# Kernel optimization log

Measured on AMD Instinct MI355X. Metric: run time of the kernel, lower is better.

Reference implementation:

```python
import jax, jax.numpy as jnp
import numpy as np

# Minimal Mamba (alxndrTL mamba.py style) as used by MambaLithium.
# d_model=512, d_inner=1024 (expand=2), d_state=16, d_conv=4, dt_rank=32, n_layers=4.

EPS = 1e-5

def rmsnorm(x, w):
    # x: (B,L,D), w: (D,)
    return x * jax.lax.rsqrt(jnp.mean(x * x, axis=-1, keepdims=True) + EPS) * w

def causal_depthwise_conv(x, w, b):
    # x: (B,L,ED), w: (ED,K), b: (ED,)
    ED, K = w.shape
    xc = jnp.swapaxes(x, 1, 2)                       # (B,ED,L)
    k = w[:, None, :]                                # (ED,1,K) OIH
    y = jax.lax.conv_general_dilated(
        xc, k, window_strides=(1,), padding=[(K - 1, 0)],
        dimension_numbers=('NCH', 'OIH', 'NCH'), feature_group_count=ED)
    return jnp.swapaxes(y + b[None, :, None], 1, 2)  # (B,L,ED)

def selective_scan(xb, delta, Bm, Cm, A, D):
    # xb, delta: (B,L,ED); Bm, Cm: (B,L,N); A: (ED,N); D: (ED,)
    def step(h, inp):
        xt, dt, bt, ct = inp                          # (B,ED),(B,ED),(B,N),(B,N)
        dA = jnp.exp(dt[:, :, None] * A)              # (B,ED,N)
        dBx = (dt * xt)[:, :, None] * bt[:, None, :]  # (B,ED,N)
        h = dA * h + dBx
        y = jnp.einsum('ben,bn->be', h, ct)
        return h, y
    B_, _, ED = xb.shape
    N = A.shape[1]
    h0 = jnp.zeros((B_, ED, N), xb.dtype)
    xs = (jnp.swapaxes(xb, 0, 1), jnp.swapaxes(delta, 0, 1),
          jnp.swapaxes(Bm, 0, 1), jnp.swapaxes(Cm, 0, 1))
    _, ys = jax.lax.scan(step, h0, xs)                # ys: (L,B,ED)
    return jnp.swapaxes(ys, 0, 1) + xb * D

def mamba_block(x, in_w, conv_w, conv_b, xproj_w, dt_w, dt_b, A_log, Dp, out_w, dt_rank, d_state):
    # x: (B,L,D)
    xz = x @ in_w.T                                   # (B,L,2*ED)
    xb, z = jnp.split(xz, 2, axis=-1)
    xb = jax.nn.silu(causal_depthwise_conv(xb, conv_w, conv_b))
    dbc = xb @ xproj_w.T                              # (B,L,R+2N)
    dt, Bm, Cm = jnp.split(dbc, [dt_rank, dt_rank + d_state], axis=-1)
    delta = jax.nn.softplus(dt @ dt_w.T + dt_b)       # (B,L,ED)
    A = -jnp.exp(A_log)                               # (ED,N)
    y = selective_scan(xb, delta, Bm, Cm, A, Dp)
    y = y * jax.nn.silu(z)
    return y @ out_w.T                                # (B,L,D)

def reference(x, fc1_w, fc1_b, fc2_w, fc2_b, norm_w, in_proj_w, conv_w, conv_b,
              xproj_w, dtproj_w, dtproj_b, A_log, D_param, out_proj_w):
    n_layers = norm_w.shape[0]
    dt_rank = dtproj_w.shape[2]
    d_state = A_log.shape[2]
    h = x @ fc1_w.T + fc1_b                           # (B,L,D)
    for i in range(n_layers):
        h = h + mamba_block(rmsnorm(h, norm_w[i]), in_proj_w[i], conv_w[i], conv_b[i],
                            xproj_w[i], dtproj_w[i], dtproj_b[i], A_log[i], D_param[i],
                            out_proj_w[i], dt_rank, d_state)
    out = jax.nn.sigmoid(h @ fc2_w.T + fc2_b)         # (B,L,out_dim)
    return out.reshape(-1)

def setup_inputs() -> dict:
    key = jax.random.key(0)
    ks = jax.random.split(key, 12)
    B, L, Din, D, Dout, NL = 4, 1024, 32, 512, 1, 4
    ED, N, K, R = 1024, 16, 4, 32
    def rn(k, shape, scale):
        return jax.random.normal(k, shape, jnp.float32) * scale
    return {
        'x': jax.random.normal(ks[0], (B, L, Din), jnp.float32),
        'fc1_w': rn(ks[1], (D, Din), 0.1),
        'fc1_b': jnp.zeros((D,), jnp.float32),
        'fc2_w': rn(ks[2], (Dout, D), 0.1),
        'fc2_b': jnp.zeros((Dout,), jnp.float32),
        'norm_w': jnp.ones((NL, D), jnp.float32),
        'in_proj_w': rn(ks[3], (NL, 2 * ED, D), 0.02),
        'conv_w': rn(ks[4], (NL, ED, K), 0.2),
        'conv_b': jnp.zeros((NL, ED), jnp.float32),
        'xproj_w': rn(ks[5], (NL, R + 2 * N, ED), 0.02),
        'dtproj_w': rn(ks[6], (NL, ED, R), 0.1),
        'dtproj_b': rn(ks[7], (NL, ED), 0.1),
        'A_log': jnp.tile(jnp.log(jnp.arange(1, N + 1, dtype=jnp.float32))[None, None, :], (NL, ED, 1)),
        'D_param': jnp.ones((NL, ED), jnp.float32),
        'out_proj_w': rn(ks[8], (NL, D, ED), 0.02),
    }
```

## Files before the change

### kernel.cpp

```cpp
#include <hip/hip_runtime.h>
#include <hip/hip_bf16.h>
#include <cmath>

#define BB 4
#define LSEQ 1024
#define DIN 32
#define DM 512
#define EDIM 1024
#define NST 16
#define RANK 32
#define MTOK (BB*LSEQ)
#define NC 32
#define CH (LSEQ/NC)
#define MB 1048576ull

typedef __attribute__((ext_vector_type(8))) short bx8;
typedef __attribute__((ext_vector_type(4))) float fx4;
typedef __hip_bfloat16 bf;

__device__ __forceinline__ float sigmoidf_(float x){ return 1.f/(1.f+__expf(-x)); }
__device__ __forceinline__ float softplusf_(float x){ return fmaxf(x,0.f) + log1pf(__expf(-fabsf(x))); }
__device__ __forceinline__ float siluf_(float x){ return x * sigmoidf_(x); }

template<int BM, int BN, int EPI>
__global__ __launch_bounds__(256) void gemm_k(const float* __restrict__ A,
    const float* __restrict__ W, const float* __restrict__ bias,
    float* __restrict__ C, int M, int N, int K, int lda, int ldw, int ldc)
{
  constexpr int BK = 16;
  constexpr int TX = BN/4;
  constexpr int TY = 256/TX;
  constexpr int TM = BM/TY;
  __shared__ float As[BK][BM];
  __shared__ float Ws[BK][BN];
  const int t = threadIdx.x;
  const int n0 = blockIdx.x*BN, m0 = blockIdx.y*BM;
  const int tx = t % TX, ty = t / TX;
  float acc[TM][4];
  #pragma unroll
  for (int i=0;i<TM;i++){ acc[i][0]=0.f;acc[i][1]=0.f;acc[i][2]=0.f;acc[i][3]=0.f; }

  for (int k0=0;k0<K;k0+=BK) {
    __syncthreads();
    for (int f=t; f<BM*4; f+=256) {
      int row=f>>2, kq=f&3;
      float4 v = *(const float4*)(A + (size_t)(m0+row)*lda + (k0+kq*4));
      As[kq*4+0][row]=v.x; As[kq*4+1][row]=v.y; As[kq*4+2][row]=v.z; As[kq*4+3][row]=v.w;
    }
    for (int f=t; f<BN*4; f+=256) {
      int row=f>>2, kq=f&3;
      float4 v = *(const float4*)(W + (size_t)(n0+row)*ldw + (k0+kq*4));
      Ws[kq*4+0][row]=v.x; Ws[kq*4+1][row]=v.y; Ws[kq*4+2][row]=v.z; Ws[kq*4+3][row]=v.w;
    }
    __syncthreads();
    #pragma unroll
    for (int kk=0;kk<BK;kk++) {
      float a[TM], b[4];
      #pragma unroll
      for (int j=0;j<4;j++) b[j] = Ws[kk][tx*4+j];
      #pragma unroll
      for (int i=0;i<TM;i++) a[i] = As[kk][ty*TM+i];
      #pragma unroll
      for (int i=0;i<TM;i++)
        #pragma unroll
        for (int j=0;j<4;j++) acc[i][j] = fmaf(a[i], b[j], acc[i][j]);
    }
  }
  #pragma unroll
  for (int i=0;i<TM;i++) {
    float* cp = C + (size_t)(m0+ty*TM+i)*ldc + n0 + tx*4;
    float4 r; r.x=acc[i][0]; r.y=acc[i][1]; r.z=acc[i][2]; r.w=acc[i][3];
    if constexpr (EPI==2) { const float* bp = bias + n0 + tx*4;
      r.x+=bp[0]; r.y+=bp[1]; r.z+=bp[2]; r.w+=bp[3]; }
    if constexpr (EPI==3) { const float* bp = bias + n0 + tx*4;
      r.x=softplusf_(r.x+bp[0]); r.y=softplusf_(r.y+bp[1]);
      r.z=softplusf_(r.z+bp[2]); r.w=softplusf_(r.w+bp[3]); }
    *(float4*)cp = r;
  }
}

template<int BM, int BN, int WR, int WC, int EPI>
__global__ __launch_bounds__(256) void gemm_mfma_k(
    const bf* __restrict__ Ahi, const bf* __restrict__ Alo,
    const bf* __restrict__ Whi, const bf* __restrict__ Wlo,
    float* __restrict__ C, int M, int N, int K)
{
  constexpr int BK = 32;
  constexpr int LDT = BK + 8;
  constexpr int WM = BM/WR, WN = BN/WC;
  constexpr int FM = WM/16, FN = WN/16;
  constexpr int CA = BM*4/256, CW = BN*4/256;
  __shared__ bf At[2][BM*LDT];
  __shared__ bf Wt[2][BN*LDT];
  const int t = threadIdx.x;
  const int w = t>>6, lane = t&63;
  const int wr = w%WR, wc = w/WR;
  const int lr = lane&15, lk = lane>>4;
  const int m0 = blockIdx.y*BM, n0 = blockIdx.x*BN;

  fx4 acc[FM][FN];
  #pragma unroll
  for (int i=0;i<FM;i++)
    #pragma unroll
    for (int j=0;j<FN;j++) acc[i][j] = fx4{0.f,0.f,0.f,0.f};

  for (int k0=0;k0<K;k0+=BK) {
    __syncthreads();
    #pragma unroll
    for (int q=0;q<CA;q++) {
      int c = q*256+t, row = c>>2, ko = (c&3)*8;
      size_t g = (size_t)(m0+row)*K + k0 + ko;
      float4 vh = *(const float4*)(Ahi+g);
      float4 vl = *(const float4*)(Alo+g);
      *(float4*)&At[0][row*LDT+ko] = vh;
      *(float4*)&At[1][row*LDT+ko] = vl;
    }
    #pragma unroll
    for (int q=0;q<CW;q++) {
      int c = q*256+t, row = c>>2, ko = (c&3)*8;
      size_t g = (size_t)(n0+row)*K + k0 + ko;
      float4 vh = *(const float4*)(Whi+g);
      float4 vl = *(const float4*)(Wlo+g);
      *(float4*)&Wt[0][row*LDT+ko] = vh;
      *(float4*)&Wt[1][row*LDT+ko] = vl;
    }
    __syncthreads();
    bx8 ah[FM], al[FM], bh[FN], bl[FN];
    #pragma unroll
    for (int i=0;i<FM;i++) {
      int row = wr*WM + i*16 + lr;
      ah[i] = *(const bx8*)&At[0][row*LDT + lk*8];
      al[i] = *(const bx8*)&At[1][row*LDT + lk*8];
    }
    #pragma unroll
    for (int j=0;j<FN;j++) {
      int row = wc*WN + j*16 + lr;
      bh[j] = *(const bx8*)&Wt[0][row*LDT + lk*8];
      bl[j] = *(const bx8*)&Wt[1][row*LDT + lk*8];
    }
    #pragma unroll
    for (int i=0;i<FM;i++)
      #pragma unroll
      for (int j=0;j<FN;j++) {
        acc[i][j] = __builtin_amdgcn_mfma_f32_16x16x32_bf16(ah[i], bh[j], acc[i][j], 0,0,0);
        acc[i][j] = __builtin_amdgcn_mfma_f32_16x16x32_bf16(ah[i], bl[j], acc[i][j], 0,0,0);
        acc[i][j] = __builtin_amdgcn_mfma_f32_16x16x32_bf16(al[i], bh[j], acc[i][j], 0,0,0);
      }
  }
  #pragma unroll
  for (int i=0;i<FM;i++)
    #pragma unroll
    for (int j=0;j<FN;j++) {
      int col = n0 + wc*WN + j*16 + lr;
      #pragma unroll
      for (int r=0;r<4;r++) {
        int row = m0 + wr*WM + i*16 + lk*4 + r;
        if constexpr (EPI==1) C[(size_t)row*N+col] += acc[i][j][r];
        else                  C[(size_t)row*N+col]  = acc[i][j][r];
      }
    }
}

__global__ __launch_bounds__(256) void split_k(const float* __restrict__ in,
    bf* __restrict__ hi, bf* __restrict__ lo, int n4)
{
  int i = blockIdx.x*256 + threadIdx.x;
  if (i >= n4) return;
  float4 v = ((const float4*)in)[i];
  float f[4] = {v.x, v.y, v.z, v.w};
  bf hh[4], ll[4];
  #pragma unroll
  for (int j=0;j<4;j++) {
    hh[j] = __float2bfloat16(f[j]);
    ll[j] = __float2bfloat16(f[j] - __bfloat162float(hh[j]));
  }
  *(float2*)(hi + 4*(size_t)i) = *(float2*)hh;
  *(float2*)(lo + 4*(size_t)i) = *(float2*)ll;
}

__global__ __launch_bounds__(256) void rmsnorm_k(const float* __restrict__ h,
    const float* __restrict__ nw, bf* __restrict__ hn_hi, bf* __restrict__ hn_lo)
{
  int m = blockIdx.x, t = threadIdx.x;
  const float* row = h + (size_t)m*DM;
  float v0 = row[t], v1 = row[t+256];
  float s = v0*v0 + v1*v1;
  #pragma unroll
  for (int off=32; off>=1; off>>=1) s += __shfl_xor(s, off, 64);
  __shared__ float red[4];
  if ((t&63)==0) red[t>>6] = s;
  __syncthreads();
  float tot = red[0]+red[1]+red[2]+red[3];
  float r = rsqrtf(tot*(1.0f/512.0f) + 1e-5f);
  float o0 = v0*r*nw[t], o1 = v1*r*nw[t+256];
  bf h0 = __float2bfloat16(o0), h1 = __float2bfloat16(o1);
  hn_hi[(size_t)m*DM+t]     = h0;
  hn_lo[(size_t)m*DM+t]     = __float2bfloat16(o0 - __bfloat162float(h0));
  hn_hi[(size_t)m*DM+t+256] = h1;
  hn_lo[(size_t)m*DM+t+256] = __float2bfloat16(o1 - __bfloat162float(h1));
}

__global__ __launch_bounds__(256) void conv_silu_k(const float* __restrict__ Xb,
    const float* __restrict__ cw, const float* __restrict__ cb, float* __restrict__ xbc)
{
  int idx = blockIdx.x*256 + threadIdx.x;
  int e = idx & (EDIM-1);
  int m = idx >> 10;
  int l = m & (LSEQ-1);
  float4 w = *(const float4*)(cw + e*4);
  const float* xp = Xb + (size_t)m*EDIM + e;
  float acc = cb[e] + w.w * xp[0];
  if (l>0) acc += w.z * xp[-EDIM];
  if (l>1) acc += w.y * xp[-2*EDIM];
  if (l>2) acc += w.x * xp[-3*EDIM];
  xbc[idx] = siluf_(acc);
}

__global__ __launch_bounds__(256) void wtrans_k(const float* __restrict__ W, float* __restrict__ Wt)
{
  __shared__ float tile[64][65];
  int kb = blockIdx.x;
  for (int i=threadIdx.x; i<4096; i+=256) {
    int n = i>>6, c = i&63;
    tile[n][c] = W[(size_t)n*EDIM + kb*64 + c];
  }
  __syncthreads();
  for (int i=threadIdx.x; i<4096; i+=256) {
    int kk = i>>6, n = i&63;
    Wt[((size_t)kb*64+kk)*64 + n] = tile[n][kk];
  }
}

__global__ __launch_bounds__(256) void xproj_part_k(const float* __restrict__ A,
    const float* __restrict__ Wt, float* __restrict__ Cp)
{
  constexpr int KC = 256;
  __shared__ float As[16][KC];
  const int mb = blockIdx.x;
  const int kc = blockIdx.y;
  const int t  = threadIdx.x;
  const float* ap = A + ((size_t)mb*16)*EDIM + kc*KC;
  #pragma unroll
  for (int q=0;q<4;q++) {
    int i = q*256 + t;
    int r = i>>6, c4 = i&63;
    float4 v = *(const float4*)(ap + (size_t)r*EDIM + c4*4);
    *(float4*)&As[r][c4*4] = v;
  }
  __syncthreads();
  const int m = t>>4, n0 = (t&15)*4;
  const float* wp = Wt + (size_t)kc*KC*64 + n0;
  float4 acc = {0.f,0.f,0.f,0.f};
  #pragma unroll 8
  for (int k=0;k<KC;k++) {
    float a = As[m][k];
    float4 w = *(const float4*)(wp + (size_t)k*64);
    acc.x = fmaf(a,w.x,acc.x); acc.y = fmaf(a,w.y,acc.y);
    acc.z = fmaf(a,w.z,acc.z); acc.w = fmaf(a,w.w,acc.w);
  }
  *(float4*)(Cp + ((size_t)kc*MTOK + (size_t)mb*16 + m)*64 + n0) = acc;
}

__global__ __launch_bounds__(256) void xproj_red_k(const float* __restrict__ Cp,
    float* __restrict__ C)
{
  int i = blockIdx.x*256 + threadIdx.x;
  const size_t stride = (size_t)MTOK*64/4;
  float4 a = ((const float4*)Cp)[i];
  float4 b = ((const float4*)Cp)[i + stride];
  float4 c = ((const float4*)Cp)[i + 2*stride];
  float4 d = ((const float4*)Cp)[i + 3*stride];
  float4 r; r.x=a.x+b.x+c.x+d.x; r.y=a.y+b.y+c.y+d.y;
  r.z=a.z+b.z+c.z+d.z; r.w=a.w+b.w+c.w+d.w;
  ((float4*)C)[i] = r;
}

__global__ __launch_bounds__(256,2) void scan_chunkA_k(const float* __restrict__ xbc,
    const float* __restrict__ dl, const float* __restrict__ dbc,
    const float* __restrict__ A_log,
    float* __restrict__ P, float* __restrict__ S)
{
  int ed = blockIdx.x*256 + threadIdx.x;
  int b = blockIdx.y, c = blockIdx.z;
  const int l0 = c*CH;
  __shared__ float Bs[CH][NST];
  for (int i=threadIdx.x; i<CH*NST; i+=256) {
    int row = i>>4, col = i&15;
    Bs[row][col] = dbc[((size_t)b*LSEQ + l0 + row)*64 + 32 + col];
  }
  __syncthreads();
  const float* dp = dl  + ((size_t)b*LSEQ + l0)*EDIM + ed;
  const float* xp = xbc + ((size_t)b*LSEQ + l0)*EDIM + ed;
  float dt[CH], xv[CH];
  #pragma unroll
  for (int l=0;l<CH;l++){ dt[l]=dp[(size_t)l*EDIM]; xv[l]=xp[(size_t)l*EDIM]; }
  float a[NST], hs[NST], pp[NST];
  #pragma unroll
  for (int n=0;n<NST;n++){ a[n] = -__expf(A_log[ed*NST+n]); hs[n]=0.f; pp[n]=1.f; }
  #pragma unroll
  for (int l=0;l<CH;l++) {
    float dx = dt[l]*xv[l];
    #pragma unroll
    for (int n=0;n<NST;n++) {
      float dA = __expf(dt[l]*a[n]);
      hs[n] = fmaf(dA, hs[n], dx*Bs[l][n]);
      pp[n] *= dA;
    }
  }
  size_t base = (((size_t)b*NC + c)*NST)*EDIM + ed;
  #pragma unroll
  for (int n=0;n<NST;n++) { P[base + (size_t)n*EDIM] = pp[n]; S[base + (size_t)n*EDIM] = hs[n]; }
}

__global__ __launch_bounds__(256) void scan_combine_k(float* __restrict__ PH, const float* __restrict__ S)
{
  int t = blockIdx.x*256 + threadIdx.x;
  int b = blockIdx.y;
  const size_t stride = (size_t)NST*EDIM;
  size_t b0 = (size_t)b*NC*stride + t;
  float p[NC], s[NC];
  #pragma unroll
  for (int c=0;c<NC;c++){ p[c]=PH[b0+(size_t)c*stride]; s[c]=S[b0+(size_t)c*stride]; }
  float H = 0.f;
  #pragma unroll
  for (int c=0;c<NC;c++){ PH[b0+(size_t)c*stride] = H; H = fmaf(p[c], H, s[c]); }
}

__global__ __launch_bounds__(256,2) void scan_chunkC_k(const float* __restrict__ xbc,
    const float* __restrict__ dl, const float* __restrict__ dbc,
    const float* __restrict__ A_log, const float* __restrict__ Dp,
    const float* __restrict__ Hinit, const float* __restrict__ Z,
    bf* __restrict__ yz_hi, bf* __restrict__ yz_lo)
{
  int ed = blockIdx.x*256 + threadIdx.x;
  int b = blockIdx.y, c = blockIdx.z;
  const int l0 = c*CH;
  __shared__ float BCs[CH][32];
  for (int i=threadIdx.x; i<CH*32; i+=256) {
    int row = i>>5, col = i&31;
    BCs[row][col] = dbc[((size_t)b*LSEQ + l0 + row)*64 + 32 + col];
  }
  __syncthreads();
  const float* dp = dl  + ((size_t)b*LSEQ + l0)*EDIM + ed;
  const float* xp = xbc + ((size_t)b*LSEQ + l0)*EDIM + ed;
  const float* zp = Z   + ((size_t)b*LSEQ + l0)*EDIM + ed;
  float dt[CH], xv[CH], zv[CH];
  #pragma unroll
  for (int l=0;l<CH;l++){ dt[l]=dp[(size_t)l*EDIM]; xv[l]=xp[(size_t)l*EDIM]; zv[l]=zp[(size_t)l*EDIM]; }
  float a[NST], hs[NST];
  size_t base = (((size_t)b*NC + c)*NST)*EDIM + ed;
  #pragma unroll
  for (int n=0;n<NST;n++){ a[n] = -__expf(A_log[ed*NST+n]); hs[n] = Hinit[base + (size_t)n*EDIM]; }
  float Dv = Dp[ed];
  bf* yh = yz_hi + ((size_t)b*LSEQ + l0)*EDIM + ed;
  bf* yl = yz_lo + ((size_t)b*LSEQ + l0)*EDIM + ed;
  #pragma unroll
  for (int l=0;l<CH;l++) {
    float dx = dt[l]*xv[l];
    float yv = xv[l]*Dv;
    #pragma unroll
    for (int n=0;n<NST;n++) {
      float dA = __expf(dt[l]*a[n]);
      hs[n] = fmaf(dA, hs[n], dx*BCs[l][n]);
      yv = fmaf(hs[n], BCs[l][16+n], yv);
    }
    float g = yv * siluf_(zv[l]);
    bf gh = __float2bfloat16(g);
    yh[(size_t)l*EDIM] = gh;
    yl[(size_t)l*EDIM] = __float2bfloat16(g - __bfloat162float(gh));
  }
}

__global__ __launch_bounds__(64) void fc2_k(const float* __restrict__ h,
    const float* __restrict__ w, const float* __restrict__ b, float* __restrict__ out)
{
  int m = blockIdx.x, t = threadIdx.x;
  float s = 0.f;
  #pragma unroll
  for (int j=0;j<8;j++) { int k = t + j*64; s = fmaf(h[(size_t)m*DM+k], w[k], s); }
  #pragma unroll
  for (int off=32; off>=1; off>>=1) s += __shfl_xor(s, off, 64);
  if (t==0) out[m] = sigmoidf_(s + b[0]);
}

extern "C" void kernel_launch(void* const* d_in, const int* in_sizes, int n_in,
                              void* d_out, int out_size, void* d_ws, size_t ws_size,
                              hipStream_t stream) {
  const float* x         = (const float*)d_in[0];
  const float* fc1_w     = (const float*)d_in[1];
  const float* fc1_b     = (const float*)d_in[2];
  const float* fc2_w     = (const float*)d_in[3];
  const float* fc2_b     = (const float*)d_in[4];
  const float* norm_w    = (const float*)d_in[5];
  const float* in_proj_w = (const float*)d_in[6];
  const float* conv_w    = (const float*)d_in[7];
  const float* conv_b    = (const float*)d_in[8];
  const float* xproj_w   = (const float*)d_in[9];
  const float* dtproj_w  = (const float*)d_in[10];
  const float* dtproj_b  = (const float*)d_in[11];
  const float* A_log     = (const float*)d_in[12];
  const float* D_param   = (const float*)d_in[13];
  const float* out_proj_w= (const float*)d_in[14];
  float* out = (float*)d_out;

  char* w8 = (char*)d_ws;
  float* h    = (float*)(w8 +  0*MB);
  float* Xb   = (float*)(w8 +  8*MB);
  float* PH   = (float*)(w8 +  8*MB);
  float* Z    = (float*)(w8 + 24*MB);
  float* xbc  = (float*)(w8 + 40*MB);
  float* dl   = (float*)(w8 + 56*MB);
  float* dbcw = (float*)(w8 + 72*MB);
  bf*    win_hi = (bf*)(w8 + 73*MB);
  float* Wt     = (float*)(w8 + 73*MB);
  bf*    win_lo = (bf*)(w8 + 75*MB);
  bf*    wout_hi= (bf*)(w8 + 77*MB);
  bf*    wout_lo= (bf*)(w8 + 78*MB);
  bf*    hn_hi  = (bf*)(w8 + 79*MB);
  bf*    hn_lo  = (bf*)(w8 + 83*MB);
  float* Send   = (float*)(w8 + 79*MB);
  float* Cp     = (float*)(w8 + 79*MB);
  bf*    yz_hi  = (bf*)(w8 + 87*MB);
  bf*    yz_lo  = (bf*)(w8 + 95*MB);

  gemm_k<128,64,2><<<dim3(DM/64, MTOK/128), 256, 0, stream>>>(
      x, fc1_w, fc1_b, h, MTOK, DM, DIN, DIN, DIN, DM);

  for (int i=0;i<4;i++) {
    rmsnorm_k<<<MTOK, 256, 0, stream>>>(h, norm_w + (size_t)i*DM, hn_hi, hn_lo);
    split_k<<<(2048*512/4)/256, 256, 0, stream>>>(
        in_proj_w + (size_t)i*2048*DM, win_hi, win_lo, 2048*512/4);
    gemm_mfma_k<128,128,2,2,0><<<dim3(EDIM/128, MTOK/128), 256, 0, stream>>>(
        hn_hi, hn_lo, win_hi, win_lo, Xb, MTOK, EDIM, DM);
    gemm_mfma_k<128,128,2,2,0><<<dim3(EDIM/128, MTOK/128), 256, 0, stream>>>(
        hn_hi, hn_lo, win_hi + (size_t)EDIM*DM, win_lo + (size_t)EDIM*DM, Z, MTOK, EDIM, DM);
    conv_silu_k<<<(MTOK*EDIM)/256, 256, 0, stream>>>(
        Xb, conv_w + (size_t)i*EDIM*4, conv_b + (size_t)i*EDIM, xbc);
    wtrans_k<<<16, 256, 0, stream>>>(xproj_w + (size_t)i*64*EDIM, Wt);
    xproj_part_k<<<dim3(MTOK/16, 4), 256, 0, stream>>>(xbc, Wt, Cp);
    xproj_red_k<<<(MTOK*64/4)/256, 256, 0, stream>>>(Cp, dbcw);
    gemm_k<128,64,3><<<dim3(EDIM/64, MTOK/128), 256, 0, stream>>>(
        dbcw, dtproj_w + (size_t)i*EDIM*RANK, dtproj_b + (size_t)i*EDIM, dl,
        MTOK, EDIM, RANK, 64, RANK, EDIM);
    scan_chunkA_k<<<dim3(EDIM/256, BB, NC), 256, 0, stream>>>(
        xbc, dl, dbcw, A_log + (size_t)i*EDIM*NST, PH, Send);
    scan_combine_k<<<dim3(NST*EDIM/256, BB), 256, 0, stream>>>(PH, Send);
    scan_chunkC_k<<<dim3(EDIM/256, BB, NC), 256, 0, stream>>>(
        xbc, dl, dbcw, A_log + (size_t)i*EDIM*NST, D_param + (size_t)i*EDIM, PH,
        Z, yz_hi, yz_lo);
    split_k<<<(512*1024/4)/256, 256, 0, stream>>>(
        out_proj_w + (size_t)i*DM*EDIM, wout_hi, wout_lo, 512*1024/4);
    gemm_mfma_k<128,64,4,1,1><<<dim3(DM/64, MTOK/128), 256, 0, stream>>>(
        yz_hi, yz_lo, wout_hi, wout_lo, h, MTOK, DM, EDIM);
  }

  fc2_k<<<MTOK, 64, 0, stream>>>(h, fc2_w, fc2_b, out);
}
```

Baseline: 1.036 ms.

## Use direct global-to-LDS loads in MFMA GEMM and fuse in_proj launches

Rewrites the split-bf16 MFMA GEMM to stage tiles with global_load_lds (16-byte direct-to-LDS loads) instead of register round-trips. It adds an XCD-aware block remap, merges the two in_proj GEMMs into one launch that routes columns to the Xb or Z buffer, and retiles the out_proj GEMM to 64x64. The goal is less load latency and register pressure, fewer launches, and better L2 locality. The unpadded LDS layout (stride 32) may cause bank conflicts on fragment reads.

```diff
diff --git a/kernel.cpp b/kernel.cpp
--- a/kernel.cpp
+++ b/kernel.cpp
@@ -22,6 +22,12 @@
 __device__ __forceinline__ float softplusf_(float x){ return fmaxf(x,0.f) + log1pf(__expf(-fabsf(x))); }
 __device__ __forceinline__ float siluf_(float x){ return x * sigmoidf_(x); }
 
+__device__ __forceinline__ void gl16(const bf* g, bf* l) {
+  __builtin_amdgcn_global_load_lds(
+      (const __attribute__((address_space(1))) void*)g,
+      (__attribute__((address_space(3))) void*)l, 16, 0, 0);
+}
+
 template<int BM, int BN, int EPI>
 __global__ __launch_bounds__(256) void gemm_k(const float* __restrict__ A,
     const float* __restrict__ W, const float* __restrict__ bias,
@@ -80,23 +86,26 @@
 }
 
 template<int BM, int BN, int WR, int WC, int EPI>
-__global__ __launch_bounds__(256) void gemm_mfma_k(
+__global__ __launch_bounds__(256) void gemm_mfma2_k(
     const bf* __restrict__ Ahi, const bf* __restrict__ Alo,
     const bf* __restrict__ Whi, const bf* __restrict__ Wlo,
-    float* __restrict__ C, int M, int N, int K)
-{
-  constexpr int BK = 32;
-  constexpr int LDT = BK + 8;
+    float* __restrict__ Cx, float* __restrict__ Cz, int nsplit,
+    int M, int N, int K, int ldc)
+{
   constexpr int WM = BM/WR, WN = BN/WC;
   constexpr int FM = WM/16, FN = WN/16;
-  constexpr int CA = BM*4/256, CW = BN*4/256;
-  __shared__ bf At[2][BM*LDT];
-  __shared__ bf Wt[2][BN*LDT];
+  __shared__ bf sAh[BM*32], sAl[BM*32], sWh[BN*32], sWl[BN*32];
   const int t = threadIdx.x;
   const int w = t>>6, lane = t&63;
   const int wr = w%WR, wc = w/WR;
   const int lr = lane&15, lk = lane>>4;
-  const int m0 = blockIdx.y*BM, n0 = blockIdx.x*BN;
+  const int rowl = lane>>2, coll = (lane&3)*8;
+
+  const int gx = gridDim.x;
+  const int flat = blockIdx.y*gx + blockIdx.x;
+  const int cpx = (gx*gridDim.y)>>3;
+  const int logical = (flat&7)*cpx + (flat>>3);
+  const int m0 = (logical/gx)*BM, n0 = (logical%gx)*BN;
 
   fx4 acc[FM][FN];
   #pragma unroll
@@ -104,39 +113,41 @@
     #pragma unroll
     for (int j=0;j<FN;j++) acc[i][j] = fx4{0.f,0.f,0.f,0.f};
 
-  for (int k0=0;k0<K;k0+=BK) {
+  for (int k0=0;k0<K;k0+=32) {
     __syncthreads();
-    #pragma unroll
-    for (int q=0;q<CA;q++) {
-      int c = q*256+t, row = c>>2, ko = (c&3)*8;
-      size_t g = (size_t)(m0+row)*K + k0 + ko;
-      float4 vh = *(const float4*)(Ahi+g);
-      float4 vl = *(const float4*)(Alo+g);
-      *(float4*)&At[0][row*LDT+ko] = vh;
-      *(float4*)&At[1][row*LDT+ko] = vl;
-    }
-    #pragma unroll
-    for (int q=0;q<CW;q++) {
-      int c = q*256+t, row = c>>2, ko = (c&3)*8;
-      size_t g = (size_t)(n0+row)*K + k0 + ko;
-      float4 vh = *(const float4*)(Whi+g);
-      float4 vl = *(const float4*)(Wlo+g);
-      *(float4*)&Wt[0][row*LDT+ko] = vh;
-      *(float4*)&Wt[1][row*LDT+ko] = vl;
+    {
+      const int rb = w*(BM/4);
+      #pragma unroll
+      for (int q=0;q<BM/64;q++) {
+        int r = rb + q*16 + rowl;
+        size_t g = (size_t)(m0+r)*K + k0 + coll;
+        gl16(Ahi+g, &sAh[(rb+q*16)*32]);
+        gl16(Alo+g, &sAl[(rb+q*16)*32]);
+      }
+    }
+    {
+      const int rb = w*(BN/4);
+      #pragma unroll
+      for (int q=0;q<BN/64;q++) {
+        int r = rb + q*16 + rowl;
+        size_t g = (size_t)(n0+r)*K + k0 + coll;
+        gl16(Whi+g, &sWh[(rb+q*16)*32]);
+        gl16(Wlo+g, &sWl[(rb+q*16)*32]);
+      }
     }
     __syncthreads();
     bx8 ah[FM], al[FM], bh[FN], bl[FN];
     #pragma unroll
     for (int i=0;i<FM;i++) {
       int row = wr*WM + i*16 + lr;
-      ah[i] = *(const bx8*)&At[0][row*LDT + lk*8];
-      al[i] = *(const bx8*)&At[1][row*LDT + lk*8];
+      ah[i] = *(const bx8*)&sAh[row*32 + lk*8];
+      al[i] = *(const bx8*)&sAl[row*32 + lk*8];
     }
     #pragma unroll
     for (int j=0;j<FN;j++) {
       int row = wc*WN + j*16 + lr;
-      bh[j] = *(const bx8*)&Wt[0][row*LDT + lk*8];
-      bl[j] = *(const bx8*)&Wt[1][row*LDT + lk*8];
+      bh[j] = *(const bx8*)&sWh[row*32 + lk*8];
+      bl[j] = *(const bx8*)&sWl[row*32 + lk*8];
     }
     #pragma unroll
     for (int i=0;i<FM;i++)
@@ -148,17 +159,20 @@
       }
   }
   #pragma unroll
-  for (int i=0;i<FM;i++)
-    #pragma unroll
-    for (int j=0;j<FN;j++) {
-      int col = n0 + wc*WN + j*16 + lr;
+  for (int j=0;j<FN;j++) {
+    int coln = n0 + wc*WN + j*16 + lr;
+    float* Cb; int cc;
+    if (coln < nsplit) { Cb = Cx; cc = coln; } else { Cb = Cz; cc = coln - nsplit; }
+    #pragma unroll
+    for (int i=0;i<FM;i++) {
       #pragma unroll
       for (int r=0;r<4;r++) {
         int row = m0 + wr*WM + i*16 + lk*4 + r;
-        if constexpr (EPI==1) C[(size_t)row*N+col] += acc[i][j][r];
-        else                  C[(size_t)row*N+col]  = acc[i][j][r];
+        if constexpr (EPI==1) Cb[(size_t)row*ldc+cc] += acc[i][j][r];
+        else                  Cb[(size_t)row*ldc+cc]  = acc[i][j][r];
       }
     }
+  }
 }
 
 __global__ __launch_bounds__(256) void split_k(const float* __restrict__ in,
@@ -430,10 +444,8 @@
     rmsnorm_k<<<MTOK, 256, 0, stream>>>(h, norm_w + (size_t)i*DM, hn_hi, hn_lo);
     split_k<<<(2048*512/4)/256, 256, 0, stream>>>(
         in_proj_w + (size_t)i*2048*DM, win_hi, win_lo, 2048*512/4);
-    gemm_mfma_k<128,128,2,2,0><<<dim3(EDIM/128, MTOK/128), 256, 0, stream>>>(
-        hn_hi, hn_lo, win_hi, win_lo, Xb, MTOK, EDIM, DM);
-    gemm_mfma_k<128,128,2,2,0><<<dim3(EDIM/128, MTOK/128), 256, 0, stream>>>(
-        hn_hi, hn_lo, win_hi + (size_t)EDIM*DM, win_lo + (size_t)EDIM*DM, Z, MTOK, EDIM, DM);
+    gemm_mfma2_k<128,128,2,2,0><<<dim3(2048/128, MTOK/128), 256, 0, stream>>>(
+        hn_hi, hn_lo, win_hi, win_lo, Xb, Z, 1024, MTOK, 2048, DM, EDIM);
     conv_silu_k<<<(MTOK*EDIM)/256, 256, 0, stream>>>(
         Xb, conv_w + (size_t)i*EDIM*4, conv_b + (size_t)i*EDIM, xbc);
     wtrans_k<<<16, 256, 0, stream>>>(xproj_w + (size_t)i*64*EDIM, Wt);
@@ -450,8 +462,8 @@
         Z, yz_hi, yz_lo);
     split_k<<<(512*1024/4)/256, 256, 0, stream>>>(
         out_proj_w + (size_t)i*DM*EDIM, wout_hi, wout_lo, 512*1024/4);
-    gemm_mfma_k<128,64,4,1,1><<<dim3(DM/64, MTOK/128), 256, 0, stream>>>(
-        yz_hi, yz_lo, wout_hi, wout_lo, h, MTOK, DM, EDIM);
+    gemm_mfma2_k<64,64,2,2,1><<<dim3(DM/64, MTOK/64), 256, 0, stream>>>(
+        yz_hi, yz_lo, wout_hi, wout_lo, h, h, DM, MTOK, DM, EDIM, DM);
   }
 
   fc2_k<<<MTOK, 64, 0, stream>>>(h, fc2_w, fc2_b, out);
```

After: 884.3 us. 1.17x faster.
